# Optimization experiments

Measured on AMD Instinct MI355X. Metric: run time of the kernel, lower is better.

## Reference

```python
import jax, jax.numpy as jnp
import numpy as np

D = 1024
H = 16
B = 8
N = 1024


def setup_inputs() -> dict:
    key = jax.random.key(0)
    k1, k2, k3 = jax.random.split(key, 3)
    x = jax.random.normal(k1, (B, N, D), dtype=jnp.float32)
    w_in = jax.random.normal(k2, (D, 3 * D), dtype=jnp.float32) * (1.0 / np.sqrt(D))
    w_out = jax.random.normal(k3, (D, D), dtype=jnp.float32) * (1.0 / np.sqrt(D))
    b_out = jnp.zeros((D,), dtype=jnp.float32)
    return {"x": x, "w_in": w_in, "w_out": w_out, "b_out": b_out}


def reference(x, w_in, w_out, b_out):
    h = H
    d = D // H
    scale = D ** (-0.5)  # note: full dimension, per source
    qkv = x @ w_in  # [B, N, 3D]
    # rearrange 'b n (qkv h d) -> qkv b h n d'
    qkv = qkv.reshape(x.shape[0], x.shape[1], 3, h, d)
    qkv = jnp.transpose(qkv, (2, 0, 3, 1, 4))
    q, k, v = qkv[0], qkv[1], qkv[2]
    scores = jnp.einsum('bhid,bhjd->bhij', q, k) * scale
    attn = jax.nn.softmax(scores, axis=-1)
    out = jnp.einsum('bhij,bhjd->bhid', attn, v)
    # 'b h n d -> b n (h d)'
    out = jnp.transpose(out, (0, 2, 1, 3)).reshape(x.shape[0], x.shape[1], h * d)
    return out @ w_out + b_out
```

## Files before the change

kernel.cpp:

```cpp
#include <hip/hip_runtime.h>
#include <stdint.h>
#include <stddef.h>

typedef __bf16 bf16;
typedef __bf16 bf16x4 __attribute__((ext_vector_type(4)));
typedef __bf16 bf16x8 __attribute__((ext_vector_type(8)));
typedef float  f32x4  __attribute__((ext_vector_type(4)));
typedef float  f32x4v __attribute__((ext_vector_type(4)));

__device__ __forceinline__ void gload_lds16(const void* g, void* lds) {
  __builtin_amdgcn_global_load_lds(
      (__attribute__((address_space(1))) void*)(uintptr_t)g,
      (__attribute__((address_space(3))) void*)lds,
      16, 0, 0);
}


__global__ void cvt_f32_to_bf16(const float* __restrict__ in, bf16* __restrict__ out, int n) {
  int i = (blockIdx.x * blockDim.x + threadIdx.x) * 4;
  if (i >= n) return;
  f32x4v v = *reinterpret_cast<const f32x4v*>(in + i);
  bf16x4 o;
  o[0] = (bf16)v[0]; o[1] = (bf16)v[1]; o[2] = (bf16)v[2]; o[3] = (bf16)v[3];
  *reinterpret_cast<bf16x4*>(out + i) = o;
}

__global__ void transpose_cvt(const float* __restrict__ in, bf16* __restrict__ out, int R, int C) {
  __shared__ bf16 tile[32][33];
  int c0 = blockIdx.x * 32, r0 = blockIdx.y * 32;
  int tx = threadIdx.x, ty = threadIdx.y;
  #pragma unroll
  for (int i = ty; i < 32; i += 8)
    tile[i][tx] = (bf16)in[(size_t)(r0 + i) * C + (c0 + tx)];
  __syncthreads();
  #pragma unroll
  for (int i = ty; i < 32; i += 8)
    out[(size_t)(c0 + i) * R + (r0 + tx)] = tile[tx][i];
}


template <typename OT, bool BIAS>
__global__ __launch_bounds__(256) void gemm_abt(
    const bf16* __restrict__ A,
    const bf16* __restrict__ Bt,
    const float* __restrict__ bias,
    OT* __restrict__ C, int M, int N, int K)
{
  __shared__ bf16 As[128 * 64];
  __shared__ bf16 Bs[128 * 64];

  const int tid = threadIdx.x;
  const int w = tid >> 6, l = tid & 63;
  const int l15 = l & 15, l4 = l >> 4, l7 = l & 7;
  const int wr = w >> 1, wc = w & 1;
  const int m0 = blockIdx.y * 128, n0 = blockIdx.x * 128;

  f32x4 acc[4][4];
  #pragma unroll
  for (int i = 0; i < 4; i++)
    #pragma unroll
    for (int j = 0; j < 4; j++) acc[i][j] = (f32x4){0.f, 0.f, 0.f, 0.f};

  const int srow  = w * 8 + (l >> 3);
  const int sslot = (l & 7) ^ ((l >> 3) & 7);
  const int KT = K >> 6;

  for (int kt = 0; kt < KT; ++kt) {
    __syncthreads();
    const int kcol = kt * 64 + sslot * 8;
    #pragma unroll
    for (int p = 0; p < 4; ++p) {
      gload_lds16(A  + (size_t)(m0 + p * 32 + srow) * K + kcol,
                  (char*)As + p * 4096 + w * 1024);
      gload_lds16(Bt + (size_t)(n0 + p * 32 + srow) * K + kcol,
                  (char*)Bs + p * 4096 + w * 1024);
    }
    __syncthreads();

    #pragma unroll
    for (int kk = 0; kk < 2; ++kk) {
      const int coff = (kk * 32 + l4 * 8) ^ (l7 << 3);
      bf16x8 af[4], bq[4];
      #pragma unroll
      for (int m = 0; m < 4; ++m) {
        int r = wr * 64 + m * 16 + l15;
        af[m] = *reinterpret_cast<const bf16x8*>(&As[r * 64 + coff]);
      }
      #pragma unroll
      for (int n = 0; n < 4; ++n) {
        int r = wc * 64 + n * 16 + l15;
        bq[n] = *reinterpret_cast<const bf16x8*>(&Bs[r * 64 + coff]);
      }
      #pragma unroll
      for (int m = 0; m < 4; ++m)
        #pragma unroll
        for (int n = 0; n < 4; ++n)
          acc[m][n] = __builtin_amdgcn_mfma_f32_16x16x32_bf16(af[m], bq[n], acc[m][n], 0, 0, 0);
    }
  }

  #pragma unroll
  for (int m = 0; m < 4; ++m) {
    #pragma unroll
    for (int n = 0; n < 4; ++n) {
      int col = n0 + wc * 64 + n * 16 + l15;
      float bv = BIAS ? bias[col] : 0.f;
      #pragma unroll
      for (int j = 0; j < 4; ++j) {
        int row = m0 + wr * 64 + m * 16 + l4 * 4 + j;
        float v = acc[m][n][j] + bv;
        C[(size_t)row * N + col] = (OT)v;
      }
    }
  }
}


__global__ __launch_bounds__(256) void attn_fused(
    const bf16* __restrict__ qkv,
    bf16* __restrict__ aout)
{
  __shared__ bf16 Ks[64 * 64];
  __shared__ bf16 Vt[64 * 64];
  __shared__ bf16 Pl[4][32 * 64];

  const int tid = threadIdx.x;
  const int w = tid >> 6, l = tid & 63;
  const int l15 = l & 15, l4 = l >> 4, l7 = l & 7;

  const int bid = blockIdx.x;
  const int c  = bid & 7, rr = bid >> 3;
  const int g  = c * 16 + (rr & 15);
  const int qt = rr >> 4;
  const int h  = g & 15;
  const int b  = g >> 4;

  const bf16* base = qkv + (size_t)b * 1024 * 3072;
  const int qrow0 = qt * 128 + w * 32;

  const float qscale = 0.03125f * 1.44269504f;
  bf16x8 qa[2][2];
  #pragma unroll
  for (int mi = 0; mi < 2; mi++)
    #pragma unroll
    for (int kk = 0; kk < 2; kk++) {
      const bf16* p = base + (size_t)(qrow0 + mi * 16 + l15) * 3072 + h * 64 + kk * 32 + l4 * 8;
      bf16x8 v = *reinterpret_cast<const bf16x8*>(p);
      #pragma unroll
      for (int e = 0; e < 8; e++) v[e] = (bf16)((float)v[e] * qscale);
      qa[mi][kk] = v;
    }

  f32x4 acc[2][4];
  #pragma unroll
  for (int i = 0; i < 2; i++)
    #pragma unroll
    for (int t = 0; t < 4; t++) acc[i][t] = (f32x4){0.f, 0.f, 0.f, 0.f};
  float lsum[2] = {0.f, 0.f};

  const int skey  = w * 8 + (l >> 3);
  const int sslot = (l & 7) ^ ((l >> 3) & 7);
  const int vd0   = (tid & 15) * 4;
  const int vk0   = (tid >> 4) * 4;
  const int vslot = tid >> 5;
  const int vhalf = (tid >> 4) & 1;

  for (int kt = 0; kt < 16; ++kt) {
    __syncthreads();
    #pragma unroll
    for (int p = 0; p < 2; ++p)
      gload_lds16(base + (size_t)(kt * 64 + p * 32 + skey) * 3072 + 1024 + h * 64 + sslot * 8,
                  (char*)Ks + p * 4096 + w * 1024);
    {
      bf16x4 vv[4];
      #pragma unroll
      for (int i = 0; i < 4; ++i)
        vv[i] = *reinterpret_cast<const bf16x4*>(
            base + (size_t)(kt * 64 + vk0 + i) * 3072 + 2048 + h * 64 + vd0);
      #pragma unroll
      for (int j = 0; j < 4; ++j) {
        int d = vd0 + j;
        bf16x4 o; o[0] = vv[0][j]; o[1] = vv[1][j]; o[2] = vv[2][j]; o[3] = vv[3][j];
        *reinterpret_cast<bf16x4*>(&Vt[d * 64 + ((vslot ^ (d & 7)) * 8 + vhalf * 4)]) = o;
      }
    }
    __syncthreads();

    f32x4 s[4][2];
    #pragma unroll
    for (int n = 0; n < 4; n++)
      #pragma unroll
      for (int mi = 0; mi < 2; mi++) s[n][mi] = (f32x4){0.f, 0.f, 0.f, 0.f};
    #pragma unroll
    for (int kk = 0; kk < 2; kk++) {
      const int coff = (kk * 32 + l4 * 8) ^ (l7 << 3);
      bf16x8 kb[4];
      #pragma unroll
      for (int n = 0; n < 4; n++) {
        int key = n * 16 + l15;
        kb[n] = *reinterpret_cast<const bf16x8*>(&Ks[key * 64 + coff]);
      }
      #pragma unroll
      for (int n = 0; n < 4; n++)
        #pragma unroll
        for (int mi = 0; mi < 2; mi++)
          s[n][mi] = __builtin_amdgcn_mfma_f32_16x16x32_bf16(kb[n], qa[mi][kk], s[n][mi], 0, 0, 0);
    }

    #pragma unroll
    for (int mi = 0; mi < 2; mi++) {
      const int prow = mi * 16 + l15;
      bf16* pbase = &Pl[w][prow * 64];
      #pragma unroll
      for (int n = 0; n < 4; n++) {
        bf16x4 pb;
        float ps = 0.f;
        #pragma unroll
        for (int r = 0; r < 4; r++) {
          float pv = exp2f(s[n][mi][r]);
          ps += pv;
          pb[r] = (bf16)pv;
        }
        lsum[mi] += ps;
        const int slot16 = 2 * n + (l4 >> 1);
        *reinterpret_cast<bf16x4*>(&pbase[((slot16 ^ l7) * 8 + (l4 & 1) * 4)]) = pb;
      }
    }

    #pragma unroll
    for (int kk = 0; kk < 2; kk++) {
      const int coff = (kk * 32 + l4 * 8) ^ (l7 << 3);
      bf16x8 pa[2];
      #pragma unroll
      for (int mi = 0; mi < 2; mi++) {
        int prow = mi * 16 + l15;
        pa[mi] = *reinterpret_cast<const bf16x8*>(&Pl[w][prow * 64 + coff]);
      }
      #pragma unroll
      for (int t = 0; t < 4; t++) {
        int d = t * 16 + l15;
        bf16x8 vb = *reinterpret_cast<const bf16x8*>(&Vt[d * 64 + coff]);
        #pragma unroll
        for (int mi = 0; mi < 2; mi++)
          acc[mi][t] = __builtin_amdgcn_mfma_f32_16x16x32_bf16(pa[mi], vb, acc[mi][t], 0, 0, 0);
      }
    }
  }

  float rinv[2][4];
  #pragma unroll
  for (int mi = 0; mi < 2; mi++) {
    float t = lsum[mi];
    t += __shfl_xor(t, 16);
    t += __shfl_xor(t, 32);
    #pragma unroll
    for (int r = 0; r < 4; r++) {
      float tt = __shfl(t, (l & 48) | (l4 * 4 + r));
      rinv[mi][r] = 1.0f / tt;
    }
  }

  #pragma unroll
  for (int mi = 0; mi < 2; mi++)
    #pragma unroll
    for (int t = 0; t < 4; t++)
      #pragma unroll
      for (int r = 0; r < 4; r++) {
        int row = qrow0 + mi * 16 + l4 * 4 + r;
        int col = h * 64 + t * 16 + l15;
        aout[((size_t)b * 1024 + row) * 1024 + col] = (bf16)(acc[mi][t][r] * rinv[mi][r]);
      }
}


extern "C" void kernel_launch(void* const* d_in, const int* in_sizes, int n_in,
                              void* d_out, int out_size, void* d_ws, size_t ws_size,
                              hipStream_t stream) {
  const float* x     = (const float*)d_in[0];
  const float* w_in  = (const float*)d_in[1];
  const float* w_out = (const float*)d_in[2];
  const float* b_out = (const float*)d_in[3];
  float* out = (float*)d_out;

  bf16* xb    = (bf16*)d_ws;
  bf16* wint  = xb    + (size_t)8192 * 1024;
  bf16* woutt = wint  + (size_t)3072 * 1024;
  bf16* qkv   = woutt + (size_t)1024 * 1024;
  bf16* ao    = qkv   + (size_t)8192 * 3072;

  cvt_f32_to_bf16<<<8192, 256, 0, stream>>>(x, xb, 8192 * 1024);
  transpose_cvt<<<dim3(96, 32), dim3(32, 8), 0, stream>>>(w_in,  wint,  1024, 3072);
  transpose_cvt<<<dim3(32, 32), dim3(32, 8), 0, stream>>>(w_out, woutt, 1024, 1024);

  gemm_abt<bf16, false><<<dim3(24, 64), 256, 0, stream>>>(xb, wint, nullptr, qkv, 8192, 3072, 1024);

  attn_fused<<<1024, 256, 0, stream>>>(qkv, ao);

  gemm_abt<float, true><<<dim3(8, 64), 256, 0, stream>>>(ao, woutt, b_out, out, 8192, 1024, 1024);
}
```

Measured before the change: 191.2 us.

## Switch attention kernel from 16x16x32 to 32x32x16 bf16 MFMA tiles

The fused attention kernel now uses 32x32x16 MFMA instructions for both the QK^T and PV products, instead of 16x16x32. The Q fragments, the swizzled P staging layout in LDS, the V fragment loads and the softmax-sum reduction and output store are all reworked to match the 32-lane row mapping. The larger tile means fewer MFMA issues and fewer LDS fragment loads per key tile. In exchange it uses larger accumulator registers and a different output store pattern.

```diff
diff --git a/kernel.cpp b/kernel.cpp
--- a/kernel.cpp
+++ b/kernel.cpp
@@ -6,6 +6,7 @@
 typedef __bf16 bf16x4 __attribute__((ext_vector_type(4)));
 typedef __bf16 bf16x8 __attribute__((ext_vector_type(8)));
 typedef float  f32x4  __attribute__((ext_vector_type(4)));
+typedef float  f32x16 __attribute__((ext_vector_type(16)));
 typedef float  f32x4v __attribute__((ext_vector_type(4)));
 
 __device__ __forceinline__ void gload_lds16(const void* g, void* lds) {
@@ -126,7 +127,7 @@
 
   const int tid = threadIdx.x;
   const int w = tid >> 6, l = tid & 63;
-  const int l15 = l & 15, l4 = l >> 4, l7 = l & 7;
+  const int l31 = l & 31, hi = l >> 5;
 
   const int bid = blockIdx.x;
   const int c  = bid & 7, rr = bid >> 3;
@@ -139,24 +140,18 @@
   const int qrow0 = qt * 128 + w * 32;
 
   const float qscale = 0.03125f * 1.44269504f;
-  bf16x8 qa[2][2];
-  #pragma unroll
-  for (int mi = 0; mi < 2; mi++)
-    #pragma unroll
-    for (int kk = 0; kk < 2; kk++) {
-      const bf16* p = base + (size_t)(qrow0 + mi * 16 + l15) * 3072 + h * 64 + kk * 32 + l4 * 8;
-      bf16x8 v = *reinterpret_cast<const bf16x8*>(p);
-      #pragma unroll
-      for (int e = 0; e < 8; e++) v[e] = (bf16)((float)v[e] * qscale);
-      qa[mi][kk] = v;
-    }
-
-  f32x4 acc[2][4];
-  #pragma unroll
-  for (int i = 0; i < 2; i++)
-    #pragma unroll
-    for (int t = 0; t < 4; t++) acc[i][t] = (f32x4){0.f, 0.f, 0.f, 0.f};
-  float lsum[2] = {0.f, 0.f};
+  bf16x8 qf[4];
+  #pragma unroll
+  for (int st = 0; st < 4; st++) {
+    const bf16* p = base + (size_t)(qrow0 + l31) * 3072 + h * 64 + st * 16 + hi * 8;
+    bf16x8 v = *reinterpret_cast<const bf16x8*>(p);
+    #pragma unroll
+    for (int e = 0; e < 8; e++) v[e] = (bf16)((float)v[e] * qscale);
+    qf[st] = v;
+  }
+
+  f32x16 acc0 = {}, acc1 = {};
+  float lsum = 0.f;
 
   const int skey  = w * 8 + (l >> 3);
   const int sslot = (l & 7) ^ ((l >> 3) & 7);
@@ -186,90 +181,52 @@
     }
     __syncthreads();
 
-    f32x4 s[4][2];
-    #pragma unroll
-    for (int n = 0; n < 4; n++)
-      #pragma unroll
-      for (int mi = 0; mi < 2; mi++) s[n][mi] = (f32x4){0.f, 0.f, 0.f, 0.f};
-    #pragma unroll
-    for (int kk = 0; kk < 2; kk++) {
-      const int coff = (kk * 32 + l4 * 8) ^ (l7 << 3);
-      bf16x8 kb[4];
-      #pragma unroll
-      for (int n = 0; n < 4; n++) {
-        int key = n * 16 + l15;
-        kb[n] = *reinterpret_cast<const bf16x8*>(&Ks[key * 64 + coff]);
-      }
-      #pragma unroll
-      for (int n = 0; n < 4; n++)
+    #pragma unroll
+    for (int ktile = 0; ktile < 2; ++ktile) {
+      f32x16 s = {};
+      const int key = ktile * 32 + l31;
+      #pragma unroll
+      for (int st = 0; st < 4; ++st) {
+        const int slot = (2 * st + hi) ^ (key & 7);
+        bf16x8 kf = *reinterpret_cast<const bf16x8*>(&Ks[key * 64 + slot * 8]);
+        s = __builtin_amdgcn_mfma_f32_32x32x16_bf16(kf, qf[st], s, 0, 0, 0);
+      }
+      #pragma unroll
+      for (int gq = 0; gq < 4; ++gq) {
+        bf16x4 pb;
         #pragma unroll
-        for (int mi = 0; mi < 2; mi++)
-          s[n][mi] = __builtin_amdgcn_mfma_f32_16x16x32_bf16(kb[n], qa[mi][kk], s[n][mi], 0, 0, 0);
-    }
-
-    #pragma unroll
-    for (int mi = 0; mi < 2; mi++) {
-      const int prow = mi * 16 + l15;
-      bf16* pbase = &Pl[w][prow * 64];
-      #pragma unroll
-      for (int n = 0; n < 4; n++) {
-        bf16x4 pb;
-        float ps = 0.f;
-        #pragma unroll
-        for (int r = 0; r < 4; r++) {
-          float pv = exp2f(s[n][mi][r]);
-          ps += pv;
-          pb[r] = (bf16)pv;
+        for (int j2 = 0; j2 < 4; ++j2) {
+          float pv = exp2f(s[4 * gq + j2]);
+          lsum += pv;
+          pb[j2] = (bf16)pv;
         }
-        lsum[mi] += ps;
-        const int slot16 = 2 * n + (l4 >> 1);
-        *reinterpret_cast<bf16x4*>(&pbase[((slot16 ^ l7) * 8 + (l4 & 1) * 4)]) = pb;
-      }
-    }
-
-    #pragma unroll
-    for (int kk = 0; kk < 2; kk++) {
-      const int coff = (kk * 32 + l4 * 8) ^ (l7 << 3);
-      bf16x8 pa[2];
-      #pragma unroll
-      for (int mi = 0; mi < 2; mi++) {
-        int prow = mi * 16 + l15;
-        pa[mi] = *reinterpret_cast<const bf16x8*>(&Pl[w][prow * 64 + coff]);
-      }
-      #pragma unroll
-      for (int t = 0; t < 4; t++) {
-        int d = t * 16 + l15;
-        bf16x8 vb = *reinterpret_cast<const bf16x8*>(&Vt[d * 64 + coff]);
-        #pragma unroll
-        for (int mi = 0; mi < 2; mi++)
-          acc[mi][t] = __builtin_amdgcn_mfma_f32_16x16x32_bf16(pa[mi], vb, acc[mi][t], 0, 0, 0);
-      }
-    }
-  }
-
-  float rinv[2][4];
-  #pragma unroll
-  for (int mi = 0; mi < 2; mi++) {
-    float t = lsum[mi];
-    t += __shfl_xor(t, 16);
-    t += __shfl_xor(t, 32);
-    #pragma unroll
-    for (int r = 0; r < 4; r++) {
-      float tt = __shfl(t, (l & 48) | (l4 * 4 + r));
-      rinv[mi][r] = 1.0f / tt;
-    }
-  }
-
-  #pragma unroll
-  for (int mi = 0; mi < 2; mi++)
-    #pragma unroll
-    for (int t = 0; t < 4; t++)
-      #pragma unroll
-      for (int r = 0; r < 4; r++) {
-        int row = qrow0 + mi * 16 + l4 * 4 + r;
-        int col = h * 64 + t * 16 + l15;
-        aout[((size_t)b * 1024 + row) * 1024 + col] = (bf16)(acc[mi][t][r] * rinv[mi][r]);
-      }
+        const int chunk = ktile * 4 + gq;
+        *reinterpret_cast<bf16x4*>(
+            &Pl[w][l31 * 64 + ((chunk ^ (l31 & 7)) * 8 + hi * 4)]) = pb;
+      }
+    }
+
+    #pragma unroll
+    for (int st = 0; st < 4; ++st) {
+      const int cslot = (2 * st + hi) ^ (l31 & 7);
+      bf16x8 pa  = *reinterpret_cast<const bf16x8*>(&Pl[w][l31 * 64 + cslot * 8]);
+      bf16x8 vf0 = *reinterpret_cast<const bf16x8*>(&Vt[l31 * 64 + cslot * 8]);
+      acc0 = __builtin_amdgcn_mfma_f32_32x32x16_bf16(pa, vf0, acc0, 0, 0, 0);
+      bf16x8 vf1 = *reinterpret_cast<const bf16x8*>(&Vt[(32 + l31) * 64 + cslot * 8]);
+      acc1 = __builtin_amdgcn_mfma_f32_32x32x16_bf16(pa, vf1, acc1, 0, 0, 0);
+    }
+  }
+
+  float tf = lsum + __shfl_xor(lsum, 32);
+
+  #pragma unroll
+  for (int reg = 0; reg < 16; ++reg) {
+    int q_r = (reg & 3) + 8 * (reg >> 2) + 4 * hi;
+    float rinv = 1.0f / __shfl(tf, q_r);
+    size_t rowoff = ((size_t)b * 1024 + qrow0 + q_r) * 1024 + h * 64;
+    aout[rowoff + l31]      = (bf16)(acc0[reg] * rinv);
+    aout[rowoff + 32 + l31] = (bf16)(acc1[reg] * rinv);
+  }
 }
 
 
```

Result: faster. 186.2 us (-2.6%).
